# Performance work log

Measured on AMD Instinct MI355X. Metric: run time of the kernel, lower is better.

Reference implementation:

```python
import jax, jax.numpy as jnp
import numpy as np

NEG_SLOPE = 0.2


def gat_conv(x, src, dst, W, a_src, a_dst, b, heads, out_ch, concat):
    """PyG-style GATConv (eval mode, self-loops already appended to src/dst)."""
    N = x.shape[0]
    h = (x @ W).reshape(N, heads, out_ch)            # [N,H,C]
    alpha_s = jnp.einsum('nhc,hc->nh', h, a_src)     # [N,H]
    alpha_d = jnp.einsum('nhc,hc->nh', h, a_dst)
    e = jax.nn.leaky_relu(alpha_s[src] + alpha_d[dst], NEG_SLOPE)  # [E,H]
    # segment softmax over incoming edges per destination node
    m = jax.ops.segment_max(e, dst, num_segments=N)  # every node has a self loop
    ex = jnp.exp(e - m[dst])
    denom = jax.ops.segment_sum(ex, dst, num_segments=N)
    alpha = ex / (denom[dst] + 1e-16)                # [E,H]
    msg = h[src] * alpha[:, :, None]                 # [E,H,C]
    out = jax.ops.segment_sum(msg, dst, num_segments=N)  # [N,H,C]
    if concat:
        out = out.reshape(N, heads * out_ch)
    else:
        out = out.mean(axis=1)
    return out + b


def setup_inputs() -> dict:
    key = jax.random.key(0)
    ks = jax.random.split(key, 12)
    N, E, F_IN = 100000, 3200000, 512
    H1, C1 = 8, 8           # conv1: heads=8, out=8, concat -> 64
    H2, C2 = 8, 16          # conv2: heads=8, out=num_classes=16, mean over heads
    x = jax.random.normal(ks[0], (N, F_IN), dtype=jnp.float32)
    edge_index = jax.random.randint(ks[1], (2, E), 0, N, dtype=jnp.int32)
    g = lambda k, s, fan: jax.random.normal(k, s, dtype=jnp.float32) / np.sqrt(fan)
    return {
        'x': x,
        'edge_index': edge_index,
        'W1': g(ks[2], (F_IN, H1 * C1), F_IN),
        'a_src1': g(ks[3], (H1, C1), C1),
        'a_dst1': g(ks[4], (H1, C1), C1),
        'b1': jnp.zeros((H1 * C1,), jnp.float32),
        'W2': g(ks[5], (H1 * C1, H2 * C2), H1 * C1),
        'a_src2': g(ks[6], (H2, C2), C2),
        'a_dst2': g(ks[7], (H2, C2), C2),
        'b2': jnp.zeros((C2,), jnp.float32),
    }


def reference(x, edge_index, W1, a_src1, a_dst1, b1, W2, a_src2, a_dst2, b2):
    N = x.shape[0]
    loops = jnp.arange(N, dtype=edge_index.dtype)
    src = jnp.concatenate([edge_index[0], loops])
    dst = jnp.concatenate([edge_index[1], loops])
    h = gat_conv(x, src, dst, W1, a_src1, a_dst1, b1, heads=8, out_ch=8, concat=True)
    h = jax.nn.elu(h)
    out = gat_conv(h, src, dst, W2, a_src2, a_dst2, b2, heads=8, out_ch=16, concat=False)
    return out
```

## Files before the change

### kernel.cpp

```cpp
#include <hip/hip_runtime.h>
#include <hip/hip_bf16.h>
#include <hip/hip_fp16.h>
#include <cstddef>

#define NEG_SLOPE 0.2f

typedef _Float16 half8 __attribute__((ext_vector_type(8)));
typedef float floatx4 __attribute__((ext_vector_type(4)));


__global__ __launch_bounds__(256) void bucket_hist_k(const int* __restrict__ dst, int E,
                                                     int* __restrict__ bhist, int NB) {
    __shared__ int lh[256];
    for (int t = threadIdx.x; t < 256; t += 256) lh[t] = 0;
    __syncthreads();
    int per = (E + gridDim.x - 1) / gridDim.x;
    int s = blockIdx.x * per;
    int e = min(s + per, E);
    for (int i = s + threadIdx.x; i < e; i += 256) atomicAdd(&lh[dst[i] >> 9], 1);
    __syncthreads();
    for (int t = threadIdx.x; t < NB; t += 256)
        if (lh[t]) atomicAdd(&bhist[t], lh[t]);
}

__global__ __launch_bounds__(256) void bucket_scan_k(const int* __restrict__ bhist, int NB,
                                                     int* __restrict__ bbase, int* __restrict__ cursor,
                                                     int* __restrict__ row_start, int N, int E) {
    __shared__ int tmp[256];
    int tid = threadIdx.x;
    int v = (tid < NB) ? bhist[tid] : 0;
    tmp[tid] = v;
    __syncthreads();
    for (int d = 1; d < 256; d <<= 1) {
        int t = tmp[tid];
        int a = (tid >= d) ? tmp[tid - d] : 0;
        __syncthreads();
        tmp[tid] = t + a;
        __syncthreads();
    }
    if (tid < NB) {
        int b = tmp[tid] - v;
        bbase[tid] = b;
        cursor[tid] = b;
    }
    if (tid == 0) {
        bbase[NB] = E;
        row_start[N] = E;
    }
}

__global__ __launch_bounds__(256) void partition_k(const int* __restrict__ src,
                                                   const int* __restrict__ dst, int E,
                                                   int* __restrict__ cursor,
                                                   unsigned int* __restrict__ part, int NB) {
    __shared__ int lh[256];
    __shared__ int lbase[256];
    for (int t = threadIdx.x; t < 256; t += 256) lh[t] = 0;
    __syncthreads();
    int per = (E + gridDim.x - 1) / gridDim.x;
    int s = blockIdx.x * per;
    int e = min(s + per, E);
    for (int i = s + threadIdx.x; i < e; i += 256) atomicAdd(&lh[dst[i] >> 9], 1);
    __syncthreads();
    for (int t = threadIdx.x; t < NB; t += 256) {
        int c = lh[t];
        lbase[t] = c ? atomicAdd(&cursor[t], c) : 0;
        lh[t] = 0;
    }
    __syncthreads();
    for (int i = s + threadIdx.x; i < e; i += 256) {
        int d = dst[i];
        int b = d >> 9;
        int lo = atomicAdd(&lh[b], 1);
        part[lbase[b] + lo] = ((unsigned)src[i] << 9) | (unsigned)(d & 511);
    }
}

__global__ __launch_bounds__(512) void bucket_build_k(const unsigned int* __restrict__ part,
                                                      const int* __restrict__ bbase,
                                                      int* __restrict__ row_start,
                                                      int* __restrict__ csr, int N) {
    __shared__ int cnt[512];
    __shared__ int cur[512];
    int b = blockIdx.x, tid = threadIdx.x;
    int n0 = b << 9;
    int s = bbase[b], e2 = bbase[b + 1];
    cnt[tid] = 0;
    __syncthreads();
    for (int i = s + tid; i < e2; i += 512) atomicAdd(&cnt[part[i] & 511], 1);
    __syncthreads();
    int v = cnt[tid];
    for (int d = 1; d < 512; d <<= 1) {
        int t = cnt[tid];
        int a = (tid >= d) ? cnt[tid - d] : 0;
        __syncthreads();
        cnt[tid] = t + a;
        __syncthreads();
    }
    int excl = cnt[tid] - v;
    if (n0 + tid < N) row_start[n0 + tid] = s + excl;
    cur[tid] = excl;
    __syncthreads();
    for (int i = s + tid; i < e2; i += 512) {
        unsigned u = part[i];
        int p = atomicAdd(&cur[u & 511], 1);
        csr[s + p] = (int)(u >> 9);
    }
}


__global__ void convw_k(const float* __restrict__ W, _Float16* __restrict__ WT,
                        int K, int Nc) {
    int i = blockIdx.x * 256 + threadIdx.x;
    if (i < K * Nc) {
        int k = i / Nc, n = i % Nc;
        WT[(size_t)n * K + k] = (_Float16)W[i];
    }
}


template <int NT, int K, bool AF32>
__global__ __launch_bounds__(256) void mfma_gemm_k(const void* __restrict__ Av,
                                                   const _Float16* __restrict__ BT,
                                                   __half* __restrict__ C, int M) {
    constexpr int Nc = NT * 16;
    int wave = threadIdx.x >> 6, lane = threadIdx.x & 63;
    int m16 = lane & 15, quad = lane >> 4;
    int arow = blockIdx.x * 64 + wave * 16 + m16;
    int arc = arow < M ? arow : M - 1;
    floatx4 acc[NT] = {};
    for (int k0 = 0; k0 < K; k0 += 32) {
        half8 af;
        if constexpr (AF32) {
            const float* ap = (const float*)Av + (size_t)arc * K + k0 + quad * 8;
            float4 v0 = *(const float4*)ap;
            float4 v1 = *(const float4*)(ap + 4);
            af[0] = (_Float16)v0.x; af[1] = (_Float16)v0.y;
            af[2] = (_Float16)v0.z; af[3] = (_Float16)v0.w;
            af[4] = (_Float16)v1.x; af[5] = (_Float16)v1.y;
            af[6] = (_Float16)v1.z; af[7] = (_Float16)v1.w;
        } else {
            af = *(const half8*)((const _Float16*)Av + (size_t)arc * K + k0 + quad * 8);
        }
#pragma unroll
        for (int t = 0; t < NT; ++t) {
            half8 bf = *(const half8*)(BT + (size_t)(t * 16 + m16) * K + k0 + quad * 8);
            acc[t] = __builtin_amdgcn_mfma_f32_16x16x32_f16(af, bf, acc[t], 0, 0, 0);
        }
    }
    int gm0 = blockIdx.x * 64 + wave * 16 + quad * 4;
#pragma unroll
    for (int t = 0; t < NT; ++t)
#pragma unroll
        for (int r = 0; r < 4; ++r) {
            int gm = gm0 + r;
            if (gm < M) C[(size_t)gm * Nc + t * 16 + m16] = __float2half(acc[t][r]);
        }
}


template <int C>
__global__ void alpha_k(const __half* __restrict__ h, const float* __restrict__ a_s,
                        const float* __restrict__ a_d, float* __restrict__ os,
                        float* __restrict__ od, int NH) {
    int i = blockIdx.x * 256 + threadIdx.x;
    if (i >= NH) return;
    int hh = i & 7;
    const __half* hp = h + (size_t)i * C;
    float s = 0.f, d = 0.f;
#pragma unroll
    for (int c = 0; c < C; ++c) {
        float v = __half2float(hp[c]);
        s = fmaf(v, a_s[hh * C + c], s);
        d = fmaf(v, a_d[hh * C + c], d);
    }
    os[i] = s;
    od[i] = d;
}


__global__ __launch_bounds__(64) void aggregate1_k(
    const __half* __restrict__ h1, const float* __restrict__ as,
    const float* __restrict__ ad, const int* __restrict__ row_start,
    const int* __restrict__ csr, const float* __restrict__ b1,
    __half* __restrict__ h1o, int N) {
    int n = blockIdx.x;
    int l = threadIdx.x;
    int h = l >> 3;
    int j = l & 7;
    int lbase = l & 56;
    float adv = ad[n * 8 + h];
    float e0 = as[n * 8 + h] + adv;
    e0 = fmaxf(e0, NEG_SLOPE * e0);
    float ex0 = __expf(e0);
    float denom = ex0;
    float acc = ex0 * __half2float(h1[(size_t)n * 64 + l]);
    int e = row_start[n], end = row_start[n + 1];
    int batched = e + ((end - e) & ~7);
    for (; e < batched; e += 8) {
        int sj = csr[e + j];
        float aj = as[sj * 8 + h];
        float t = aj + adv;
        t = fmaxf(t, NEG_SLOPE * t);
        float xj = __expf(t);
#pragma unroll
        for (int q = 0; q < 8; ++q) {
            int sq = __shfl(sj, q, 64);
            float xq = __shfl(xj, lbase + q, 64);
            float v = __half2float(h1[(size_t)sq * 64 + l]);
            denom += xq;
            acc = fmaf(xq, v, acc);
        }
    }
    for (; e < end; ++e) {
        int s0 = csr[e];
        float t = as[s0 * 8 + h] + adv;
        t = fmaxf(t, NEG_SLOPE * t);
        float x0 = __expf(t);
        denom += x0;
        acc = fmaf(x0, __half2float(h1[(size_t)s0 * 64 + l]), acc);
    }
    float v = acc / denom + b1[l];
    h1o[(size_t)n * 64 + l] = __float2half(v > 0.f ? v : expm1f(v));
}


__global__ __launch_bounds__(64) void aggregate2_k(
    const __half* __restrict__ h2, const float* __restrict__ as,
    const float* __restrict__ ad, const int* __restrict__ row_start,
    const int* __restrict__ csr, const float* __restrict__ b2,
    float* __restrict__ out, int N) {
    int n = blockIdx.x;
    int l = threadIdx.x;
    int h = l >> 3;
    int j = l & 7;
    int lbase = l & 56;
    const __half2* H = (const __half2*)h2;
    float adv = ad[n * 8 + h];
    float e0 = as[n * 8 + h] + adv;
    e0 = fmaxf(e0, NEG_SLOPE * e0);
    float ex0 = __expf(e0);
    float denom = ex0;
    float2 self = __half22float2(H[(size_t)n * 64 + l]);
    float accx = ex0 * self.x, accy = ex0 * self.y;
    int e = row_start[n], end = row_start[n + 1];
    int batched = e + ((end - e) & ~7);
    for (; e < batched; e += 8) {
        int sj = csr[e + j];
        float aj = as[sj * 8 + h];
        float t = aj + adv;
        t = fmaxf(t, NEG_SLOPE * t);
        float xj = __expf(t);
#pragma unroll
        for (int q = 0; q < 8; ++q) {
            int sq = __shfl(sj, q, 64);
            float xq = __shfl(xj, lbase + q, 64);
            float2 v = __half22float2(H[(size_t)sq * 64 + l]);
            denom += xq;
            accx = fmaf(xq, v.x, accx);
            accy = fmaf(xq, v.y, accy);
        }
    }
    for (; e < end; ++e) {
        int s0 = csr[e];
        float t = as[s0 * 8 + h] + adv;
        t = fmaxf(t, NEG_SLOPE * t);
        float x0 = __expf(t);
        float2 v = __half22float2(H[(size_t)s0 * 64 + l]);
        denom += x0;
        accx = fmaf(x0, v.x, accx);
        accy = fmaf(x0, v.y, accy);
    }
    float rx = accx / denom, ry = accy / denom;
#pragma unroll
    for (int m = 8; m <= 32; m <<= 1) {
        rx += __shfl_xor(rx, m, 64);
        ry += __shfl_xor(ry, m, 64);
    }
    if (l < 8) {
        int c0 = l * 2;
        float2 o;
        o.x = rx * 0.125f + b2[c0];
        o.y = ry * 0.125f + b2[c0 + 1];
        *(float2*)(out + (size_t)n * 16 + c0) = o;
    }
}


extern "C" void kernel_launch(void* const* d_in, const int* in_sizes, int n_in,
                              void* d_out, int out_size, void* d_ws, size_t ws_size,
                              hipStream_t stream) {
    (void)n_in; (void)out_size; (void)ws_size;
    const float* x      = (const float*)d_in[0];
    const int*   ei     = (const int*)d_in[1];
    const float* W1     = (const float*)d_in[2];
    const float* a_src1 = (const float*)d_in[3];
    const float* a_dst1 = (const float*)d_in[4];
    const float* b1     = (const float*)d_in[5];
    const float* W2     = (const float*)d_in[6];
    const float* a_src2 = (const float*)d_in[7];
    const float* a_dst2 = (const float*)d_in[8];
    const float* b2     = (const float*)d_in[9];

    int N = in_sizes[0] / 512;
    int E = in_sizes[1] / 2;
    const int* src = ei;
    const int* dst = ei + E;
    int NB = (N + 511) >> 9;

    char* ws = (char*)d_ws;
    size_t off = 0;
    auto alloc = [&](size_t bytes) -> void* {
        void* p = ws + off;
        off = (off + bytes + 255) & ~(size_t)255;
        return p;
    };
    __half* h1  = (__half*)alloc((size_t)N * 64 * 2);
    __half* h1o = (__half*)alloc((size_t)N * 64 * 2);
    __half* h2  = (__half*)alloc((size_t)N * 128 * 2);
    float* as1  = (float*)alloc((size_t)N * 8 * 4);
    float* ad1  = (float*)alloc((size_t)N * 8 * 4);
    float* as2  = (float*)alloc((size_t)N * 8 * 4);
    float* ad2  = (float*)alloc((size_t)N * 8 * 4);
    _Float16* W1T = (_Float16*)alloc((size_t)512 * 64 * 2);
    _Float16* W2T = (_Float16*)alloc((size_t)64 * 128 * 2);
    int* row_start = (int*)alloc((size_t)(N + 1) * 4);
    int* bhist     = (int*)alloc(256 * 4);
    int* bbase     = (int*)alloc(257 * 4);
    int* cursor    = (int*)alloc(256 * 4);
    unsigned int* part = (unsigned int*)alloc((size_t)E * 4);
    int* csr       = (int*)alloc((size_t)E * 4);

    convw_k<<<(512 * 64 + 255) / 256, 256, 0, stream>>>(W1, W1T, 512, 64);
    convw_k<<<(64 * 128 + 255) / 256, 256, 0, stream>>>(W2, W2T, 64, 128);

    hipMemsetAsync(bhist, 0, 256 * 4, stream);
    bucket_hist_k<<<512, 256, 0, stream>>>(dst, E, bhist, NB);
    bucket_scan_k<<<1, 256, 0, stream>>>(bhist, NB, bbase, cursor, row_start, N, E);
    partition_k<<<512, 256, 0, stream>>>(src, dst, E, cursor, part, NB);
    bucket_build_k<<<NB, 512, 0, stream>>>(part, bbase, row_start, csr, N);

    int gblocks = (N + 63) / 64;

    mfma_gemm_k<4, 512, true><<<gblocks, 256, 0, stream>>>(x, W1T, h1, N);
    alpha_k<8><<<(N * 8 + 255) / 256, 256, 0, stream>>>(h1, a_src1, a_dst1, as1, ad1, N * 8);
    aggregate1_k<<<N, 64, 0, stream>>>(h1, as1, ad1, row_start, csr, b1, h1o, N);

    mfma_gemm_k<8, 64, false><<<gblocks, 256, 0, stream>>>(h1o, W2T, h2, N);
    alpha_k<16><<<(N * 8 + 255) / 256, 256, 0, stream>>>(h2, a_src2, a_dst2, as2, ad2, N * 8);
    aggregate2_k<<<N, 64, 0, stream>>>(h2, as2, ad2, row_start, csr, b2, (float*)d_out, N);
}
```

Measured before the change: 697.4 us.

## Fuse attention logits into GEMM epilogues, store layer-2 features as FP8, two nodes per wave

```diff
diff --git a/kernel.cpp b/kernel.cpp
--- a/kernel.cpp
+++ b/kernel.cpp
@@ -7,6 +7,7 @@
 
 typedef _Float16 half8 __attribute__((ext_vector_type(8)));
 typedef float floatx4 __attribute__((ext_vector_type(4)));
+typedef float floatx2 __attribute__((ext_vector_type(2)));
 
 
 __global__ __launch_bounds__(256) void bucket_hist_k(const int* __restrict__ dst, int E,
@@ -119,29 +120,28 @@
 }
 
 
-template <int NT, int K, bool AF32>
-__global__ __launch_bounds__(256) void mfma_gemm_k(const void* __restrict__ Av,
-                                                   const _Float16* __restrict__ BT,
-                                                   __half* __restrict__ C, int M) {
-    constexpr int Nc = NT * 16;
+__global__ __launch_bounds__(256) void gemm1_k(const float* __restrict__ A,
+                                               const _Float16* __restrict__ BT,
+                                               const float* __restrict__ a_s,
+                                               const float* __restrict__ a_d,
+                                               __half* __restrict__ C,
+                                               float* __restrict__ os,
+                                               float* __restrict__ od, int M) {
+    constexpr int NT = 4, K = 512, Nc = 64;
     int wave = threadIdx.x >> 6, lane = threadIdx.x & 63;
     int m16 = lane & 15, quad = lane >> 4;
     int arow = blockIdx.x * 64 + wave * 16 + m16;
     int arc = arow < M ? arow : M - 1;
     floatx4 acc[NT] = {};
     for (int k0 = 0; k0 < K; k0 += 32) {
+        const float* ap = A + (size_t)arc * K + k0 + quad * 8;
+        float4 v0 = *(const float4*)ap;
+        float4 v1 = *(const float4*)(ap + 4);
         half8 af;
-        if constexpr (AF32) {
-            const float* ap = (const float*)Av + (size_t)arc * K + k0 + quad * 8;
-            float4 v0 = *(const float4*)ap;
-            float4 v1 = *(const float4*)(ap + 4);
-            af[0] = (_Float16)v0.x; af[1] = (_Float16)v0.y;
-            af[2] = (_Float16)v0.z; af[3] = (_Float16)v0.w;
-            af[4] = (_Float16)v1.x; af[5] = (_Float16)v1.y;
-            af[6] = (_Float16)v1.z; af[7] = (_Float16)v1.w;
-        } else {
-            af = *(const half8*)((const _Float16*)Av + (size_t)arc * K + k0 + quad * 8);
-        }
+        af[0] = (_Float16)v0.x; af[1] = (_Float16)v0.y;
+        af[2] = (_Float16)v0.z; af[3] = (_Float16)v0.w;
+        af[4] = (_Float16)v1.x; af[5] = (_Float16)v1.y;
+        af[6] = (_Float16)v1.z; af[7] = (_Float16)v1.w;
 #pragma unroll
         for (int t = 0; t < NT; ++t) {
             half8 bf = *(const half8*)(BT + (size_t)(t * 16 + m16) * K + k0 + quad * 8);
@@ -149,140 +149,180 @@
         }
     }
     int gm0 = blockIdx.x * 64 + wave * 16 + quad * 4;
-#pragma unroll
-    for (int t = 0; t < NT; ++t)
+    int head = (m16 >> 3);
+#pragma unroll
+    for (int t = 0; t < NT; ++t) {
+        float ws = a_s[(2 * t + head) * 8 + (m16 & 7)];
+        float wd = a_d[(2 * t + head) * 8 + (m16 & 7)];
 #pragma unroll
         for (int r = 0; r < 4; ++r) {
             int gm = gm0 + r;
-            if (gm < M) C[(size_t)gm * Nc + t * 16 + m16] = __float2half(acc[t][r]);
-        }
-}
-
-
-template <int C>
-__global__ void alpha_k(const __half* __restrict__ h, const float* __restrict__ a_s,
-                        const float* __restrict__ a_d, float* __restrict__ os,
-                        float* __restrict__ od, int NH) {
-    int i = blockIdx.x * 256 + threadIdx.x;
-    if (i >= NH) return;
-    int hh = i & 7;
-    const __half* hp = h + (size_t)i * C;
-    float s = 0.f, d = 0.f;
-#pragma unroll
-    for (int c = 0; c < C; ++c) {
-        float v = __half2float(hp[c]);
-        s = fmaf(v, a_s[hh * C + c], s);
-        d = fmaf(v, a_d[hh * C + c], d);
-    }
-    os[i] = s;
-    od[i] = d;
+            float v = acc[t][r];
+            if (gm < M) C[(size_t)gm * Nc + t * 16 + m16] = __float2half(v);
+            float s = v * ws, d = v * wd;
+            s += __shfl_xor(s, 1, 64); d += __shfl_xor(d, 1, 64);
+            s += __shfl_xor(s, 2, 64); d += __shfl_xor(d, 2, 64);
+            s += __shfl_xor(s, 4, 64); d += __shfl_xor(d, 4, 64);
+            if ((m16 & 7) == 0 && gm < M) {
+                os[gm * 8 + 2 * t + head] = s;
+                od[gm * 8 + 2 * t + head] = d;
+            }
+        }
+    }
+}
+
+
+__global__ __launch_bounds__(256) void gemm2_k(const _Float16* __restrict__ A,
+                                               const _Float16* __restrict__ BT,
+                                               const float* __restrict__ a_s,
+                                               const float* __restrict__ a_d,
+                                               unsigned short* __restrict__ Cf8,
+                                               float* __restrict__ os,
+                                               float* __restrict__ od, int M) {
+    constexpr int NT = 8, K = 64;
+    int wave = threadIdx.x >> 6, lane = threadIdx.x & 63;
+    int m16 = lane & 15, quad = lane >> 4;
+    int arow = blockIdx.x * 64 + wave * 16 + m16;
+    int arc = arow < M ? arow : M - 1;
+    floatx4 acc[NT] = {};
+    for (int k0 = 0; k0 < K; k0 += 32) {
+        half8 af = *(const half8*)(A + (size_t)arc * K + k0 + quad * 8);
+#pragma unroll
+        for (int t = 0; t < NT; ++t) {
+            half8 bf = *(const half8*)(BT + (size_t)(t * 16 + m16) * K + k0 + quad * 8);
+            acc[t] = __builtin_amdgcn_mfma_f32_16x16x32_f16(af, bf, acc[t], 0, 0, 0);
+        }
+    }
+    int gm0 = blockIdx.x * 64 + wave * 16 + quad * 4;
+#pragma unroll
+    for (int t = 0; t < NT; ++t) {
+        float ws = a_s[t * 16 + m16];
+        float wd = a_d[t * 16 + m16];
+#pragma unroll
+        for (int r = 0; r < 4; ++r) {
+            int gm = gm0 + r;
+            float v = acc[t][r];
+            float o = __shfl_xor(v, 1, 64);
+            if (gm < M && !(m16 & 1)) {
+                unsigned p = __builtin_amdgcn_cvt_pk_fp8_f32(v, o, 0, false);
+                Cf8[(size_t)gm * 64 + t * 8 + (m16 >> 1)] = (unsigned short)(p & 0xffff);
+            }
+            float s = v * ws, d = v * wd;
+            s += __shfl_xor(s, 1, 64); d += __shfl_xor(d, 1, 64);
+            s += __shfl_xor(s, 2, 64); d += __shfl_xor(d, 2, 64);
+            s += __shfl_xor(s, 4, 64); d += __shfl_xor(d, 4, 64);
+            s += __shfl_xor(s, 8, 64); d += __shfl_xor(d, 8, 64);
+            if (gm < M && m16 == t) {
+                os[gm * 8 + t] = s;
+                od[gm * 8 + t] = d;
+            }
+        }
+    }
 }
 
 
 __global__ __launch_bounds__(64) void aggregate1_k(
-    const __half* __restrict__ h1, const float* __restrict__ as,
+    const __half2* __restrict__ H1, const float* __restrict__ as,
     const float* __restrict__ ad, const int* __restrict__ row_start,
     const int* __restrict__ csr, const float* __restrict__ b1,
-    __half* __restrict__ h1o, int N) {
-    int n = blockIdx.x;
+    __half2* __restrict__ h1o, int N) {
     int l = threadIdx.x;
-    int h = l >> 3;
-    int j = l & 7;
-    int lbase = l & 56;
+    int ll = l & 31;
+    int n = min(blockIdx.x * 2 + (l >> 5), N - 1);
+    int h = ll >> 2;
+    int jj = ll & 3;
+    int hbase = (l & 32) | (ll & 28);
     float adv = ad[n * 8 + h];
     float e0 = as[n * 8 + h] + adv;
     e0 = fmaxf(e0, NEG_SLOPE * e0);
     float ex0 = __expf(e0);
     float denom = ex0;
-    float acc = ex0 * __half2float(h1[(size_t)n * 64 + l]);
+    float2 self = __half22float2(H1[(size_t)n * 32 + ll]);
+    float accx = ex0 * self.x, accy = ex0 * self.y;
     int e = row_start[n], end = row_start[n + 1];
-    int batched = e + ((end - e) & ~7);
-    for (; e < batched; e += 8) {
-        int sj = csr[e + j];
-        float aj = as[sj * 8 + h];
-        float t = aj + adv;
+    for (; e < end; e += 4) {
+        int rem = end - e;
+        int sj = csr[e + min(jj, rem - 1)];
+        float t = as[sj * 8 + h] + adv;
         t = fmaxf(t, NEG_SLOPE * t);
         float xj = __expf(t);
-#pragma unroll
-        for (int q = 0; q < 8; ++q) {
-            int sq = __shfl(sj, q, 64);
-            float xq = __shfl(xj, lbase + q, 64);
-            float v = __half2float(h1[(size_t)sq * 64 + l]);
+        int qmax = min(rem, 4);
+        for (int q = 0; q < qmax; ++q) {
+            int sq = __shfl(sj, hbase + q, 64);
+            float xq = __shfl(xj, hbase + q, 64);
+            float2 v = __half22float2(H1[(size_t)sq * 32 + ll]);
             denom += xq;
-            acc = fmaf(xq, v, acc);
-        }
-    }
-    for (; e < end; ++e) {
-        int s0 = csr[e];
-        float t = as[s0 * 8 + h] + adv;
-        t = fmaxf(t, NEG_SLOPE * t);
-        float x0 = __expf(t);
-        denom += x0;
-        acc = fmaf(x0, __half2float(h1[(size_t)s0 * 64 + l]), acc);
-    }
-    float v = acc / denom + b1[l];
-    h1o[(size_t)n * 64 + l] = __float2half(v > 0.f ? v : expm1f(v));
+            accx = fmaf(xq, v.x, accx);
+            accy = fmaf(xq, v.y, accy);
+        }
+    }
+    float vx = accx / denom + b1[2 * ll];
+    float vy = accy / denom + b1[2 * ll + 1];
+    vx = vx > 0.f ? vx : expm1f(vx);
+    vy = vy > 0.f ? vy : expm1f(vy);
+    h1o[(size_t)n * 32 + ll] = __floats2half2_rn(vx, vy);
 }
 
 
 __global__ __launch_bounds__(64) void aggregate2_k(
-    const __half* __restrict__ h2, const float* __restrict__ as,
+    const unsigned int* __restrict__ H2, const float* __restrict__ as,
     const float* __restrict__ ad, const int* __restrict__ row_start,
     const int* __restrict__ csr, const float* __restrict__ b2,
     float* __restrict__ out, int N) {
-    int n = blockIdx.x;
     int l = threadIdx.x;
-    int h = l >> 3;
-    int j = l & 7;
-    int lbase = l & 56;
-    const __half2* H = (const __half2*)h2;
+    int ll = l & 31;
+    int n = min(blockIdx.x * 2 + (l >> 5), N - 1);
+    int h = ll >> 2;
+    int jj = ll & 3;
+    int hbase = (l & 32) | (ll & 28);
     float adv = ad[n * 8 + h];
     float e0 = as[n * 8 + h] + adv;
     e0 = fmaxf(e0, NEG_SLOPE * e0);
     float ex0 = __expf(e0);
     float denom = ex0;
-    float2 self = __half22float2(H[(size_t)n * 64 + l]);
-    float accx = ex0 * self.x, accy = ex0 * self.y;
+    unsigned sv = H2[(size_t)n * 32 + ll];
+    floatx2 s01 = __builtin_amdgcn_cvt_pk_f32_fp8((int)sv, false);
+    floatx2 s23 = __builtin_amdgcn_cvt_pk_f32_fp8((int)sv, true);
+    float a0 = ex0 * s01[0], a1 = ex0 * s01[1];
+    float a2 = ex0 * s23[0], a3 = ex0 * s23[1];
     int e = row_start[n], end = row_start[n + 1];
-    int batched = e + ((end - e) & ~7);
-    for (; e < batched; e += 8) {
-        int sj = csr[e + j];
-        float aj = as[sj * 8 + h];
-        float t = aj + adv;
+    for (; e < end; e += 4) {
+        int rem = end - e;
+        int sj = csr[e + min(jj, rem - 1)];
+        float t = as[sj * 8 + h] + adv;
         t = fmaxf(t, NEG_SLOPE * t);
         float xj = __expf(t);
-#pragma unroll
-        for (int q = 0; q < 8; ++q) {
-            int sq = __shfl(sj, q, 64);
-            float xq = __shfl(xj, lbase + q, 64);
-            float2 v = __half22float2(H[(size_t)sq * 64 + l]);
+        int qmax = min(rem, 4);
+        for (int q = 0; q < qmax; ++q) {
+            int sq = __shfl(sj, hbase + q, 64);
+            float xq = __shfl(xj, hbase + q, 64);
+            unsigned gv = H2[(size_t)sq * 32 + ll];
+            floatx2 v01 = __builtin_amdgcn_cvt_pk_f32_fp8((int)gv, false);
+            floatx2 v23 = __builtin_amdgcn_cvt_pk_f32_fp8((int)gv, true);
             denom += xq;
-            accx = fmaf(xq, v.x, accx);
-            accy = fmaf(xq, v.y, accy);
-        }
-    }
-    for (; e < end; ++e) {
-        int s0 = csr[e];
-        float t = as[s0 * 8 + h] + adv;
-        t = fmaxf(t, NEG_SLOPE * t);
-        float x0 = __expf(t);
-        float2 v = __half22float2(H[(size_t)s0 * 64 + l]);
-        denom += x0;
-        accx = fmaf(x0, v.x, accx);
-        accy = fmaf(x0, v.y, accy);
-    }
-    float rx = accx / denom, ry = accy / denom;
-#pragma unroll
-    for (int m = 8; m <= 32; m <<= 1) {
-        rx += __shfl_xor(rx, m, 64);
-        ry += __shfl_xor(ry, m, 64);
-    }
-    if (l < 8) {
-        int c0 = l * 2;
-        float2 o;
-        o.x = rx * 0.125f + b2[c0];
-        o.y = ry * 0.125f + b2[c0 + 1];
-        *(float2*)(out + (size_t)n * 16 + c0) = o;
+            a0 = fmaf(xq, v01[0], a0);
+            a1 = fmaf(xq, v01[1], a1);
+            a2 = fmaf(xq, v23[0], a2);
+            a3 = fmaf(xq, v23[1], a3);
+        }
+    }
+    float inv = 1.f / denom;
+    a0 *= inv; a1 *= inv; a2 *= inv; a3 *= inv;
+#pragma unroll
+    for (int m = 4; m <= 16; m <<= 1) {
+        a0 += __shfl_xor(a0, m, 64);
+        a1 += __shfl_xor(a1, m, 64);
+        a2 += __shfl_xor(a2, m, 64);
+        a3 += __shfl_xor(a3, m, 64);
+    }
+    if (ll < 4) {
+        int c0 = ll * 4;
+        float4 o;
+        o.x = a0 * 0.125f + b2[c0];
+        o.y = a1 * 0.125f + b2[c0 + 1];
+        o.z = a2 * 0.125f + b2[c0 + 2];
+        o.w = a3 * 0.125f + b2[c0 + 3];
+        *(float4*)(out + (size_t)n * 16 + c0) = o;
     }
 }
 
@@ -317,7 +357,7 @@
     };
     __half* h1  = (__half*)alloc((size_t)N * 64 * 2);
     __half* h1o = (__half*)alloc((size_t)N * 64 * 2);
-    __half* h2  = (__half*)alloc((size_t)N * 128 * 2);
+    unsigned short* h2f8 = (unsigned short*)alloc((size_t)N * 64 * 2);
     float* as1  = (float*)alloc((size_t)N * 8 * 4);
     float* ad1  = (float*)alloc((size_t)N * 8 * 4);
     float* as2  = (float*)alloc((size_t)N * 8 * 4);
@@ -341,12 +381,14 @@
     bucket_build_k<<<NB, 512, 0, stream>>>(part, bbase, row_start, csr, N);
 
     int gblocks = (N + 63) / 64;
-
-    mfma_gemm_k<4, 512, true><<<gblocks, 256, 0, stream>>>(x, W1T, h1, N);
-    alpha_k<8><<<(N * 8 + 255) / 256, 256, 0, stream>>>(h1, a_src1, a_dst1, as1, ad1, N * 8);
-    aggregate1_k<<<N, 64, 0, stream>>>(h1, as1, ad1, row_start, csr, b1, h1o, N);
-
-    mfma_gemm_k<8, 64, false><<<gblocks, 256, 0, stream>>>(h1o, W2T, h2, N);
-    alpha_k<16><<<(N * 8 + 255) / 256, 256, 0, stream>>>(h2, a_src2, a_dst2, as2, ad2, N * 8);
-    aggregate2_k<<<N, 64, 0, stream>>>(h2, as2, ad2, row_start, csr, b2, (float*)d_out, N);
-}
+    int ablocks = (N + 1) / 2;
+
+    gemm1_k<<<gblocks, 256, 0, stream>>>(x, W1T, a_src1, a_dst1, h1, as1, ad1, N);
+    aggregate1_k<<<ablocks, 64, 0, stream>>>((const __half2*)h1, as1, ad1, row_start,
+                                             csr, b1, (__half2*)h1o, N);
+
+    gemm2_k<<<gblocks, 256, 0, stream>>>((const _Float16*)h1o, W2T, a_src2, a_dst2,
+                                         h2f8, as2, ad2, N);
+    aggregate2_k<<<ablocks, 64, 0, stream>>>((const unsigned int*)h2f8, as2, ad2,
+                                             row_start, csr, b2, (float*)d_out, N);
+}
```

New measurement: 762.9 us. 9.4% more time.
